# Kernel optimization log

Hardware: AMD Instinct MI355X
Metric: run time of the kernel (lower is better)

The kernel has to match this reference:

```python
import jax, jax.numpy as jnp
import numpy as np

HEADS = 16
DIM_HEAD = 64
SCALE = DIM_HEAD ** -0.5


def setup_inputs() -> dict:
    key = jax.random.key(0)
    k1, k2, k3 = jax.random.split(key, 3)
    dim, inner = 1024, HEADS * DIM_HEAD
    b, n = 2, 2048
    x = jax.random.normal(k1, (b, n, dim), dtype=jnp.float32)
    w_qkv = jax.random.normal(k2, (dim, 3 * inner), dtype=jnp.float32) * (dim ** -0.5)
    w_out = jax.random.normal(k3, (inner, dim), dtype=jnp.float32) * (inner ** -0.5)
    b_out = jnp.zeros((dim,), dtype=jnp.float32)
    return {"x": x, "w_qkv": w_qkv, "w_out": w_out, "b_out": b_out}


def reference(x, w_qkv, w_out, b_out):
    b, n, _ = x.shape
    qkv = x @ w_qkv                                   # [b,n,3*inner]
    q, k, v = jnp.split(qkv, 3, axis=-1)
    def to_heads(t):
        return t.reshape(b, n, HEADS, DIM_HEAD).transpose(0, 2, 1, 3)  # [b,h,n,d]
    q, k, v = to_heads(q), to_heads(k), to_heads(v)
    dots = jnp.einsum('bhid,bhjd->bhij', q, k) * SCALE  # [b,h,n,n]
    attn = jax.nn.softmax(dots, axis=-1)
    out = jnp.einsum('bhij,bhjd->bhid', attn, v)        # [b,h,n,d]
    out = out.transpose(0, 2, 1, 3).reshape(b, n, HEADS * DIM_HEAD)
    return out @ w_out + b_out
```

## Files before the change

kernel.cpp:

```cpp
#include <hip/hip_runtime.h>
#include <hip/hip_bf16.h>

typedef unsigned short u16;
typedef unsigned int u32;
typedef __attribute__((ext_vector_type(8))) short short8;
typedef __attribute__((ext_vector_type(4))) float f32x4;
typedef __attribute__((ext_vector_type(16))) float f32x16;
typedef __attribute__((ext_vector_type(2))) u32 u32x2;

typedef __attribute__((address_space(1))) void as1_void;
typedef __attribute__((address_space(3))) void as3_void;

__device__ __forceinline__ u16 f2b(float x) {
    union { float f; u32 u; } c; c.f = x;
    u32 r = c.u + 0x7fffu + ((c.u >> 16) & 1u);
    return (u16)(r >> 16);
}
__device__ __forceinline__ float b2f(u16 x) {
    union { u32 u; float f; } c; c.u = ((u32)x) << 16;
    return c.f;
}
__device__ __forceinline__ u32 cvtpk(float lo, float hi) {
    u32 r;
    asm("v_cvt_pk_bf16_f32 %0, %1, %2" : "=v"(r) : "v"(lo), "v"(hi));
    return r;
}
__device__ __forceinline__ void gload16(const u16* g, u16* l) {
    __builtin_amdgcn_global_load_lds((as1_void*)(u16*)g, (as3_void*)l, 16, 0, 0);
}
__device__ __forceinline__ void barrier_raw() {
    asm volatile("" ::: "memory");
    __builtin_amdgcn_s_barrier();
    asm volatile("" ::: "memory");
}

__global__ __launch_bounds__(256) void convert_cvt(const float* __restrict__ in,
                                                   u16* __restrict__ out, int n8) {
    int i = blockIdx.x * 256 + threadIdx.x;
    if (i >= n8) return;
    const float4* p = (const float4*)(in + (size_t)i * 8);
    float4 a = p[0], b = p[1];
    short8 v;
    v[0]=(short)f2b(a.x); v[1]=(short)f2b(a.y); v[2]=(short)f2b(a.z); v[3]=(short)f2b(a.w);
    v[4]=(short)f2b(b.x); v[5]=(short)f2b(b.y); v[6]=(short)f2b(b.z); v[7]=(short)f2b(b.w);
    *(short8*)(out + (size_t)i * 8) = v;
}

__global__ __launch_bounds__(256) void transpose_cvt(const float* __restrict__ in,
                                                     u16* __restrict__ out, int R, int C) {
    __shared__ u16 tile[64][72];
    const int t = threadIdx.x;
    const int r0 = blockIdx.y * 64, c0 = blockIdx.x * 64;
    {
        const int rr = t >> 2;
        const int cq = (t & 3) * 16;
        const float* src = in + (size_t)(r0 + rr) * C + c0 + cq;
        #pragma unroll
        for (int j = 0; j < 4; j++) {
            float4 v = *(const float4*)(src + j * 4);
            tile[cq + j*4 + 0][rr] = f2b(v.x);
            tile[cq + j*4 + 1][rr] = f2b(v.y);
            tile[cq + j*4 + 2][rr] = f2b(v.z);
            tile[cq + j*4 + 3][rr] = f2b(v.w);
        }
    }
    __syncthreads();
    {
        const int cc = t >> 2;
        const int rq = (t & 3) * 16;
        u16* dst = out + (size_t)(c0 + cc) * R + r0 + rq;
        *(short8*)(dst)     = *(const short8*)&tile[cc][rq];
        *(short8*)(dst + 8) = *(const short8*)&tile[cc][rq + 8];
    }
}

template<bool QKV_MODE>
__global__ __launch_bounds__(256) void gemm128(const u16* __restrict__ A,
                                               const u16* __restrict__ Bt,
                                               void* __restrict__ Cp,
                                               u16* __restrict__ vt,
                                               const float* __restrict__ bias,
                                               int M, int Nn, int K) {
    __shared__ __align__(16) u16 a_lds[2][128 * 32];
    __shared__ __align__(16) u16 b_lds[2][128 * 32];
    const int tid = threadIdx.x;
    const int w = tid >> 6, l = tid & 63;
    const int l16 = l & 15, lg = l >> 4;
    const int m0 = blockIdx.y * 128, n0 = blockIdx.x * 128;
    const int wm = w >> 1, wn = w & 1;
    const int lr = l >> 2;
    const int scol = (l & 3) * 8;

    f32x4 acc[4][4];
    #pragma unroll
    for (int i = 0; i < 4; i++)
        #pragma unroll
        for (int j = 0; j < 4; j++) { f32x4 z = {0.f,0.f,0.f,0.f}; acc[i][j] = z; }

    const u16* Ap = A  + (size_t)m0 * K;
    const u16* Bp = Bt + (size_t)n0 * K;

#define STAGE(BUF, KOF)                                                              \
    _Pragma("unroll")                                                                \
    for (int j = 0; j < 2; j++) {                                                    \
        const int r = w * 32 + j * 16;                                               \
        gload16(Ap + (size_t)(r + lr) * K + (KOF) + scol, &a_lds[(BUF)][r * 32]);    \
        gload16(Bp + (size_t)(r + lr) * K + (KOF) + scol, &b_lds[(BUF)][r * 32]);    \
    }

    const int nk = K >> 5;
    STAGE(0, 0)
    int cur = 0;
    for (int kt = 0; kt < nk; kt++) {
        if (kt + 1 < nk) {
            STAGE(cur ^ 1, (kt + 1) << 5)
            __builtin_amdgcn_sched_barrier(0);
            asm volatile("s_waitcnt vmcnt(4)" ::: "memory");
            __builtin_amdgcn_sched_barrier(0);
        } else {
            __builtin_amdgcn_sched_barrier(0);
            asm volatile("s_waitcnt vmcnt(0)" ::: "memory");
            __builtin_amdgcn_sched_barrier(0);
        }
        barrier_raw();
        short8 af[4], bf8[4];
        #pragma unroll
        for (int mb = 0; mb < 4; mb++)
            af[mb] = *(const short8*)&a_lds[cur][(wm * 64 + mb * 16 + l16) * 32 + lg * 8];
        #pragma unroll
        for (int nb = 0; nb < 4; nb++)
            bf8[nb] = *(const short8*)&b_lds[cur][(wn * 64 + nb * 16 + l16) * 32 + lg * 8];
        #pragma unroll
        for (int mb = 0; mb < 4; mb++)
            #pragma unroll
            for (int nb = 0; nb < 4; nb++)
                acc[mb][nb] = __builtin_amdgcn_mfma_f32_16x16x32_bf16(af[mb], bf8[nb], acc[mb][nb], 0, 0, 0);
        barrier_raw();
        cur ^= 1;
    }
#undef STAGE

    #pragma unroll
    for (int mb = 0; mb < 4; mb++) {
        #pragma unroll
        for (int nb = 0; nb < 4; nb++) {
            const int col = n0 + wn * 64 + nb * 16 + l16;
            const int row0 = m0 + wm * 64 + mb * 16 + lg * 4;
            if constexpr (QKV_MODE) {
                if (col < 2048) {
                    #pragma unroll
                    for (int r = 0; r < 4; r++)
                        ((u16*)Cp)[(size_t)(row0 + r) * Nn + col] = f2b(acc[mb][nb][r]);
                } else {
                    const int hd = col - 2048;
                    const int hh = hd >> 6, d = hd & 63;
                    const int bi = row0 >> 11, n = row0 & 2047;
                    u32x2 pr;
                    pr.x = cvtpk(acc[mb][nb][0], acc[mb][nb][1]);
                    pr.y = cvtpk(acc[mb][nb][2], acc[mb][nb][3]);
                    *(u32x2*)(vt + ((size_t)((bi * 16 + hh) * 64 + d)) * 2048 + n) = pr;
                }
            } else {
                #pragma unroll
                for (int r = 0; r < 4; r++)
                    ((float*)Cp)[(size_t)(row0 + r) * Nn + col] = acc[mb][nb][r] + bias[col];
            }
        }
    }
}

__global__ __launch_bounds__(512, 2) void attn_kernel(const u16* __restrict__ qkv,
                                                      const u16* __restrict__ vt,
                                                      u16* __restrict__ out) {
    __shared__ __align__(16) u16 k_lds[8192];
    __shared__ __align__(16) u16 v_lds[8192];
    const int tid = threadIdx.x;
    const int w = tid >> 6, l = tid & 63;
    const int l31 = l & 31, hi = l >> 5;
    const int bb = blockIdx.z, h = blockIdx.y;
    const int q0 = blockIdx.x * 256 + w * 32;
    const int swzl = (l31 & 7) << 3;

    const u16* qp = qkv + (size_t)(bb * 2048 + q0 + l31) * 3072 + h * 64 + hi * 8;
    short8 qf[4];
    #pragma unroll
    for (int c4 = 0; c4 < 4; c4++) {
        short8 v = *(const short8*)(qp + c4 * 16);
        #pragma unroll
        for (int e = 0; e < 8; e++) v[e] = (short)f2b(b2f((u16)v[e]) * 0.125f);
        qf[c4] = v;
    }

    f32x16 o[2];
    #pragma unroll
    for (int d0 = 0; d0 < 2; d0++)
        #pragma unroll
        for (int e = 0; e < 16; e++) o[d0][e] = 0.f;
    float mrow = -1e30f, lsum = 0.f;

    const int srow = tid >> 3, scol = tid & 7;
    const int kd = srow * 64 + ((scol ^ (srow & 7)) * 8);
    const u16* ksrc = qkv + (size_t)(bb * 2048 + srow) * 3072 + 1024 + h * 64 + scol * 8;
    const u16* vsrc = vt + (size_t)((bb * 16 + h) * 64 + srow) * 2048 + scol * 8;

    short8 krg = *(const short8*)ksrc;
    short8 vrg = *(const short8*)vsrc;
    ksrc += 64 * 3072; vsrc += 64;
    *(short8*)&k_lds[kd] = krg;
    *(short8*)&v_lds[kd] = vrg;
    __syncthreads();

#define DO_TILE(CUR, NXT)                                                               \
  {                                                                                     \
     \
    krg = *(const short8*)ksrc; vrg = *(const short8*)vsrc;                             \
    ksrc += 64 * 3072; vsrc += 64;                                                      \
    f32x16 st[2];                                                                       \
    _Pragma("unroll") for (int tt = 0; tt < 2; tt++)                                    \
      _Pragma("unroll") for (int e = 0; e < 16; e++) st[tt][e] = 0.f;                   \
    _Pragma("unroll")                                                                   \
    for (int c4 = 0; c4 < 4; c4++) {                                                    \
      short8 kf0 = *(const short8*)&k_lds[(CUR) + (l31)*64      + ((c4*16 + hi*8) ^ swzl)]; \
      short8 kf1 = *(const short8*)&k_lds[(CUR) + (32 + l31)*64 + ((c4*16 + hi*8) ^ swzl)]; \
      st[0] = __builtin_amdgcn_mfma_f32_32x32x16_bf16(kf0, qf[c4], st[0], 0, 0, 0);     \
      st[1] = __builtin_amdgcn_mfma_f32_32x32x16_bf16(kf1, qf[c4], st[1], 0, 0, 0);     \
    }                                                                                   \
    float pmax = st[0][0];                                                              \
    _Pragma("unroll") for (int e = 1; e < 16; e++) pmax = fmaxf(pmax, st[0][e]);        \
    _Pragma("unroll") for (int e = 0; e < 16; e++) pmax = fmaxf(pmax, st[1][e]);        \
    const float rowm = fmaxf(pmax, __shfl_xor(pmax, 32));                               \
    if (__any(rowm > mrow + 5.5451774f)) {              \
      const float mnew  = fmaxf(mrow, rowm);                                            \
      const float alpha = __expf(mrow - mnew);                                          \
      lsum *= alpha;                                                                    \
      _Pragma("unroll") for (int d0 = 0; d0 < 2; d0++)                                  \
        _Pragma("unroll") for (int e = 0; e < 16; e++) o[d0][e] *= alpha;               \
      mrow = mnew;                                                                      \
    }                                                                                   \
    _Pragma("unroll") for (int tt = 0; tt < 2; tt++)                                    \
      _Pragma("unroll") for (int e = 0; e < 16; e++) st[tt][e] = __expf(st[tt][e] - mrow); \
    float psum = 0.f;                                                                   \
    _Pragma("unroll") for (int tt = 0; tt < 2; tt++)                                    \
      _Pragma("unroll") for (int e = 0; e < 16; e++) psum += st[tt][e];                 \
    lsum += psum + __shfl_xor(psum, 32);                                                \
    short8 pb[4];                                                                       \
    _Pragma("unroll")                                                                   \
    for (int tt = 0; tt < 2; tt++) {                                                    \
      _Pragma("unroll")                                                                 \
      for (int g = 0; g < 2; g++) {                                                     \
         \
        u32 w0 = cvtpk(st[tt][8*g + 0], st[tt][8*g + 1]);                               \
        u32 w1 = cvtpk(st[tt][8*g + 2], st[tt][8*g + 3]);                               \
        u32 w2 = cvtpk(st[tt][8*g + 4], st[tt][8*g + 5]);                               \
        u32 w3 = cvtpk(st[tt][8*g + 6], st[tt][8*g + 7]);                               \
        u32 w0x = (u32)__shfl_xor((int)w0, 32);                                         \
        u32 w1x = (u32)__shfl_xor((int)w1, 32);                                         \
        u32 w2x = (u32)__shfl_xor((int)w2, 32);                                         \
        u32 w3x = (u32)__shfl_xor((int)w3, 32);                                         \
        union { u32 wd[4]; short8 s8; } uu;                                             \
        uu.wd[0] = hi ? w2x : w0;                                                       \
        uu.wd[1] = hi ? w3x : w1;                                                       \
        uu.wd[2] = hi ? w2  : w0x;                                                      \
        uu.wd[3] = hi ? w3  : w1x;                                                      \
        pb[2*tt + g] = uu.s8;                                                           \
      }                                                                                 \
    }                                                                                   \
    _Pragma("unroll")                                                                   \
    for (int ks = 0; ks < 4; ks++) {                                                    \
      short8 vf0 = *(const short8*)&v_lds[(CUR) + (l31)*64      + ((ks*16 + hi*8) ^ swzl)]; \
      short8 vf1 = *(const short8*)&v_lds[(CUR) + (32 + l31)*64 + ((ks*16 + hi*8) ^ swzl)]; \
      o[0] = __builtin_amdgcn_mfma_f32_32x32x16_bf16(vf0, pb[ks], o[0], 0, 0, 0);       \
      o[1] = __builtin_amdgcn_mfma_f32_32x32x16_bf16(vf1, pb[ks], o[1], 0, 0, 0);       \
    }                                                                                   \
    *(short8*)&k_lds[(NXT) + kd] = krg;                                                 \
    *(short8*)&v_lds[(NXT) + kd] = vrg;                                                 \
    __syncthreads();                                                                    \
  }

    for (int it = 0; it < 16; it++) {
        DO_TILE(0, 4096)
        DO_TILE(4096, 0)
    }
#undef DO_TILE

    const float invl = 1.0f / lsum;
    u16* op = out + (size_t)(bb * 2048 + q0 + l31) * 1024 + h * 64;
    #pragma unroll
    for (int d0 = 0; d0 < 2; d0++) {
        #pragma unroll
        for (int s = 0; s < 4; s++) {
            u32x2 pr;
            pr.x = cvtpk(o[d0][4*s + 0] * invl, o[d0][4*s + 1] * invl);
            pr.y = cvtpk(o[d0][4*s + 2] * invl, o[d0][4*s + 3] * invl);
            *(u32x2*)(op + d0 * 32 + s * 8 + hi * 4) = pr;
        }
    }
}

extern "C" void kernel_launch(void* const* d_in, const int* in_sizes, int n_in,
                              void* d_out, int out_size, void* d_ws, size_t ws_size,
                              hipStream_t stream) {
    const float* x     = (const float*)d_in[0];
    const float* w_qkv = (const float*)d_in[1];
    const float* w_out = (const float*)d_in[2];
    const float* b_out = (const float*)d_in[3];

    char* ws = (char*)d_ws;
    u16* xb    = (u16*)(ws);
    u16* wqkvT = (u16*)(ws + (size_t)( 8u << 20));
    u16* woutT = (u16*)(ws + (size_t)(14u << 20));
    u16* qkvb  = (u16*)(ws + (size_t)(16u << 20));
    u16* vtb   = (u16*)(ws + (size_t)(40u << 20));
    u16* aout  = (u16*)(ws + (size_t)(48u << 20));

    convert_cvt<<<2048, 256, 0, stream>>>(x, xb, 4096 * 1024 / 8);
    transpose_cvt<<<dim3(48, 16), 256, 0, stream>>>(w_qkv, wqkvT, 1024, 3072);
    transpose_cvt<<<dim3(16, 16), 256, 0, stream>>>(w_out, woutT, 1024, 1024);

    gemm128<true><<<dim3(24, 32), 256, 0, stream>>>(xb, wqkvT, qkvb, vtb, nullptr,
                                                    4096, 3072, 1024);
    attn_kernel<<<dim3(8, 16, 2), 512, 0, stream>>>(qkvb, vtb, aout);

    gemm128<false><<<dim3(8, 32), 256, 0, stream>>>(aout, woutT, d_out, nullptr, b_out,
                                                    4096, 1024, 1024);
}
```

Before: 128.0 us.

## Remap blocks XCD-aware and halve attention block size to 256 threads

Gemm and attention blocks are remapped so that consecutive logical tiles land on the same XCD (flat index modulo 8), with the aim of improving L2 reuse of shared B/K/V data. The attention kernel now uses 256-thread blocks covering 128 queries, giving 512 blocks instead of 256. Each thread now loads two 16-byte chunks of K and V per tile. Smaller blocks give more blocks to schedule across CUs, but each K/V tile is loaded from global memory twice as often overall.

```diff
diff --git a/kernel.cpp b/kernel.cpp
--- a/kernel.cpp
+++ b/kernel.cpp
@@ -86,7 +86,11 @@
     const int tid = threadIdx.x;
     const int w = tid >> 6, l = tid & 63;
     const int l16 = l & 15, lg = l >> 4;
-    const int m0 = blockIdx.y * 128, n0 = blockIdx.x * 128;
+    const int nbx = gridDim.x;
+    const int flat = blockIdx.x + nbx * blockIdx.y;
+    const int cpx = (nbx * gridDim.y) >> 3;
+    const int logical = (flat & 7) * cpx + (flat >> 3);
+    const int m0 = (logical / nbx) * 128, n0 = (logical % nbx) * 128;
     const int wm = w >> 1, wn = w & 1;
     const int lr = l >> 2;
     const int scol = (l & 3) * 8;
@@ -169,7 +173,7 @@
     }
 }
 
-__global__ __launch_bounds__(512, 2) void attn_kernel(const u16* __restrict__ qkv,
+__global__ __launch_bounds__(256, 2) void attn_kernel(const u16* __restrict__ qkv,
                                                       const u16* __restrict__ vt,
                                                       u16* __restrict__ out) {
     __shared__ __align__(16) u16 k_lds[8192];
@@ -177,8 +181,10 @@
     const int tid = threadIdx.x;
     const int w = tid >> 6, l = tid & 63;
     const int l31 = l & 31, hi = l >> 5;
-    const int bb = blockIdx.z, h = blockIdx.y;
-    const int q0 = blockIdx.x * 256 + w * 32;
+    const int flat = blockIdx.x + (blockIdx.y << 4) + (blockIdx.z << 8);
+    const int logical = (flat & 7) * 64 + (flat >> 3);
+    const int xq = logical & 15, h = (logical >> 4) & 15, bb = logical >> 8;
+    const int q0 = xq * 128 + w * 32;
     const int swzl = (l31 & 7) << 3;
 
     const u16* qp = qkv + (size_t)(bb * 2048 + q0 + l31) * 3072 + h * 64 + hi * 8;
@@ -198,22 +204,24 @@
         for (int e = 0; e < 16; e++) o[d0][e] = 0.f;
     float mrow = -1e30f, lsum = 0.f;
 
-    const int srow = tid >> 3, scol = tid & 7;
-    const int kd = srow * 64 + ((scol ^ (srow & 7)) * 8);
-    const u16* ksrc = qkv + (size_t)(bb * 2048 + srow) * 3072 + 1024 + h * 64 + scol * 8;
-    const u16* vsrc = vt + (size_t)((bb * 16 + h) * 64 + srow) * 2048 + scol * 8;
-
-    short8 krg = *(const short8*)ksrc;
-    short8 vrg = *(const short8*)vsrc;
+    const int srow = tid >> 2, sc = tid & 3;
+    const int kd0 = srow * 64 + ((sc ^ (srow & 7)) * 8);
+    const int kd1 = srow * 64 + (((sc + 4) ^ (srow & 7)) * 8);
+    const u16* ksrc = qkv + (size_t)(bb * 2048 + srow) * 3072 + 1024 + h * 64 + sc * 8;
+    const u16* vsrc = vt + (size_t)((bb * 16 + h) * 64 + srow) * 2048 + sc * 8;
+
+    short8 kr0 = *(const short8*)ksrc, kr1 = *(const short8*)(ksrc + 32);
+    short8 vr0 = *(const short8*)vsrc, vr1 = *(const short8*)(vsrc + 32);
     ksrc += 64 * 3072; vsrc += 64;
-    *(short8*)&k_lds[kd] = krg;
-    *(short8*)&v_lds[kd] = vrg;
+    *(short8*)&k_lds[kd0] = kr0; *(short8*)&k_lds[kd1] = kr1;
+    *(short8*)&v_lds[kd0] = vr0; *(short8*)&v_lds[kd1] = vr1;
     __syncthreads();
 
 #define DO_TILE(CUR, NXT)                                                               \
   {                                                                                     \
      \
-    krg = *(const short8*)ksrc; vrg = *(const short8*)vsrc;                             \
+    kr0 = *(const short8*)ksrc; kr1 = *(const short8*)(ksrc + 32);                      \
+    vr0 = *(const short8*)vsrc; vr1 = *(const short8*)(vsrc + 32);                      \
     ksrc += 64 * 3072; vsrc += 64;                                                      \
     f32x16 st[2];                                                                       \
     _Pragma("unroll") for (int tt = 0; tt < 2; tt++)                                    \
@@ -272,8 +280,8 @@
       o[0] = __builtin_amdgcn_mfma_f32_32x32x16_bf16(vf0, pb[ks], o[0], 0, 0, 0);       \
       o[1] = __builtin_amdgcn_mfma_f32_32x32x16_bf16(vf1, pb[ks], o[1], 0, 0, 0);       \
     }                                                                                   \
-    *(short8*)&k_lds[(NXT) + kd] = krg;                                                 \
-    *(short8*)&v_lds[(NXT) + kd] = vrg;                                                 \
+    *(short8*)&k_lds[(NXT) + kd0] = kr0; *(short8*)&k_lds[(NXT) + kd1] = kr1;           \
+    *(short8*)&v_lds[(NXT) + kd0] = vr0; *(short8*)&v_lds[(NXT) + kd1] = vr1;           \
     __syncthreads();                                                                    \
   }
 
@@ -319,7 +327,7 @@
 
     gemm128<true><<<dim3(24, 32), 256, 0, stream>>>(xb, wqkvT, qkvb, vtb, nullptr,
                                                     4096, 3072, 1024);
-    attn_kernel<<<dim3(8, 16, 2), 512, 0, stream>>>(qkvb, vtb, aout);
+    attn_kernel<<<dim3(16, 16, 2), 256, 0, stream>>>(qkvb, vtb, aout);
 
     gemm128<false><<<dim3(8, 32), 256, 0, stream>>>(aout, woutT, d_out, nullptr, b_out,
                                                     4096, 1024, 1024);
```

Result: no change. 127.6 us (-0.3%).
